# Kernel optimization log

Hardware: AMD Instinct MI355X
Metric: run time of the kernel (lower is better)

## Reference

```python
import math
import jax, jax.numpy as jnp
import numpy as np

B, S, H, N = 2, 2048, 1024, 16
HN = H // N
ALPHA = 32.0


def setup_inputs() -> dict:
    key = jax.random.key(0)
    k1, k2, k3, k4, k5 = jax.random.split(key, 5)
    hidden_states = jax.random.normal(k1, (B, S, H), dtype=jnp.float32)
    # lower-triangular causal mask, broadcastable over batch and heads
    ltor_mask = jnp.tril(jnp.ones((S, S), dtype=jnp.float32))[None, None]
    w_qkv = jax.random.normal(k2, (H, 3 * H), dtype=jnp.float32) * 0.02
    b_qkv = jax.random.normal(k3, (3 * H,), dtype=jnp.float32) * 0.02
    w_dense = jax.random.normal(k4, (H, H), dtype=jnp.float32) * 0.02
    b_dense = jax.random.normal(k5, (H,), dtype=jnp.float32) * 0.02
    return {"hidden_states": hidden_states, "ltor_mask": ltor_mask,
            "w_qkv": w_qkv, "b_qkv": b_qkv, "w_dense": w_dense, "b_dense": b_dense}


def reference(hidden_states, ltor_mask, w_qkv, b_qkv, w_dense, b_dense):
    b, s, h = hidden_states.shape
    # fused QKV projection, split into q/k/v chunks along last dim
    qkv = hidden_states @ w_qkv + b_qkv            # [b, s, 3h]
    q, k, v = jnp.split(qkv, 3, axis=-1)
    # [b, s, h] -> [b, n, s, hn]
    def heads(t):
        return t.reshape(b, s, N, HN).transpose(0, 2, 1, 3)
    q, k, v = heads(q), heads(k), heads(v)
    # pb-relax: scale q before the matmul
    scores = jnp.einsum('bnqd,bnkd->bnqk', q / math.sqrt(HN), k)  # [b, n, s, s]
    mask = ltor_mask[:, :, -s:]                    # [1, 1, s, s]
    scores = scores * mask - 10000.0 * (1.0 - mask)
    # pb-relax max-subtraction stabilization (max over both score dims per head)
    ss = scores / ALPHA
    m = jax.lax.stop_gradient(jnp.max(ss.reshape(b, N, -1), axis=-1))[:, :, None, None]
    scores = (ss - m) * ALPHA
    probs = jax.nn.softmax(scores, axis=-1)        # dropout prob = 0
    ctx = jnp.einsum('bnqk,bnkd->bnqd', probs, v)  # [b, n, s, hn]
    ctx = ctx.transpose(0, 2, 1, 3).reshape(b, s, h)
    out = ctx @ w_dense + b_dense
    return out
```

## Files before the change

### kernel.cpp

```cpp
#include <hip/hip_runtime.h>
#include <hip/hip_bf16.h>
#include <stdint.h>

#define BB 2
#define SS 2048
#define HH 1024

typedef unsigned short u16;
typedef uint32_t u32;
typedef short bf8v __attribute__((ext_vector_type(8)));
typedef float f4 __attribute__((ext_vector_type(4)));

__device__ __forceinline__ u16 f2bf(float f) {
    u32 u = __builtin_bit_cast(u32, f);
    u = (u + 0x7fffu + ((u >> 16) & 1u)) >> 16;
    return (u16)u;
}

__device__ __forceinline__ void async16(const void* g, void* lds) {
    __builtin_amdgcn_global_load_lds(
        (const __attribute__((address_space(1))) u32*)g,
        (__attribute__((address_space(3))) u32*)lds, 16, 0, 0);
}

__device__ __forceinline__ bf8v lds8(const u16* base, int byteoff) {
    return *(const bf8v*)((const char*)base + byteoff);
}

__global__ void cast_f32_bf16(const float* __restrict__ in, u16* __restrict__ out, int n) {
    int i = (blockIdx.x * blockDim.x + threadIdx.x) * 4;
    if (i < n) {
        float4 v = *(const float4*)(in + i);
        ushort4 o;
        o.x = f2bf(v.x); o.y = f2bf(v.y); o.z = f2bf(v.z); o.w = f2bf(v.w);
        *(ushort4*)(out + i) = o;
    }
}

__global__ void transpose_cast(const float* __restrict__ w, u16* __restrict__ wt, int K, int Nn) {
    __shared__ float tile[32][33];
    int tn = blockIdx.x, tk = blockIdx.y;
    int c = threadIdx.x & 31, r0 = threadIdx.x >> 5;
#pragma unroll
    for (int it = 0; it < 4; ++it) {
        int r = r0 + it * 8;
        tile[r][c] = w[(size_t)(tk * 32 + r) * Nn + tn * 32 + c];
    }
    __syncthreads();
#pragma unroll
    for (int it = 0; it < 4; ++it) {
        int r = r0 + it * 8;
        wt[(size_t)(tn * 32 + r) * K + tk * 32 + c] = f2bf(tile[c][r]);
    }
}

template<int EPI>
__global__ __launch_bounds__(256) void gemm_bt(
    const u16* __restrict__ A, const u16* __restrict__ Bt,
    const float* __restrict__ bias, void* __restrict__ Cout,
    int M, int N, int K)
{
    __shared__ __align__(16) u16 As[128 * 64];
    __shared__ __align__(16) u16 Bs[128 * 64];
    const int m0 = blockIdx.y * 128, n0 = blockIdx.x * 128;
    const int t = threadIdx.x, w = t >> 6, l = t & 63;
    const int wr = w >> 1, wc = w & 1;

    f4 acc[4][4];
#pragma unroll
    for (int i = 0; i < 4; ++i)
#pragma unroll
        for (int j = 0; j < 4; ++j) acc[i][j] = (f4){0.f, 0.f, 0.f, 0.f};

    const int nk = K >> 6;
    for (int kt = 0; kt < nk; ++kt) {
        const int k0 = kt << 6;
#pragma unroll
        for (int i = 0; i < 4; ++i) {
            int chunk = w * 256 + i * 64 + l;
            int row = chunk >> 3, seg = chunk & 7;
            int segg = seg ^ (row & 7);
            async16(A + (size_t)(m0 + row) * K + k0 + segg * 8,
                    (char*)As + (w * 256 + i * 64) * 16);
        }
#pragma unroll
        for (int i = 0; i < 4; ++i) {
            int chunk = w * 256 + i * 64 + l;
            int row = chunk >> 3, seg = chunk & 7;
            int segg = seg ^ (row & 7);
            async16(Bt + (size_t)(n0 + row) * K + k0 + segg * 8,
                    (char*)Bs + (w * 256 + i * 64) * 16);
        }
        __syncthreads();
#pragma unroll
        for (int kk = 0; kk < 2; ++kk) {
            bf8v af[4], bq[4];
#pragma unroll
            for (int fq = 0; fq < 4; ++fq) {
                int row = wr * 64 + fq * 16 + (l & 15);
                af[fq] = lds8(As, (row * 128 + kk * 64 + ((l >> 4) * 16)) ^ ((row & 7) << 4));
            }
#pragma unroll
            for (int fr = 0; fr < 4; ++fr) {
                int row = wc * 64 + fr * 16 + (l & 15);
                bq[fr] = lds8(Bs, (row * 128 + kk * 64 + ((l >> 4) * 16)) ^ ((row & 7) << 4));
            }
#pragma unroll
            for (int fq = 0; fq < 4; ++fq)
#pragma unroll
                for (int fr = 0; fr < 4; ++fr)
                    acc[fq][fr] = __builtin_amdgcn_mfma_f32_16x16x32_bf16(
                        af[fq], bq[fr], acc[fq][fr], 0, 0, 0);
        }
        __syncthreads();
    }
#pragma unroll
    for (int fq = 0; fq < 4; ++fq) {
#pragma unroll
        for (int fr = 0; fr < 4; ++fr) {
            int col = n0 + wc * 64 + fr * 16 + (l & 15);
            float bv = bias[col];
#pragma unroll
            for (int j = 0; j < 4; ++j) {
                int row = m0 + wr * 64 + fq * 16 + ((l >> 4) * 4) + j;
                float v = acc[fq][fr][j] + bv;
                if (EPI == 0) {
                    if (col < HH) v *= 0.125f;
                    ((u16*)Cout)[(size_t)row * N + col] = f2bf(v);
                } else {
                    ((float*)Cout)[(size_t)row * N + col] = v;
                }
            }
        }
    }
}

__global__ __launch_bounds__(256) void attn_kernel(
    const u16* __restrict__ qkv,
    u16* __restrict__ ctx)
{
    __shared__ __align__(16) u16 Ks[2][64 * 64];
    __shared__ __align__(16) u16 Vt[2][64 * 64];
    __shared__ __align__(16) u16 Ps[4][16 * 64];

    const int bid = blockIdx.x;
    const int head = (bid & 7) * 4 + (bid >> 7);
    const int p    = (bid >> 3) & 15;
    const int b = head >> 4, n = head & 15;
    const int w = threadIdx.x >> 6, l = threadIdx.x & 63;
    const size_t rs = 3072;

    const int qtA = p, qtB = 31 - p;
    const int ntA = qtA + 1;
    const int S_TOT = 33;

    const u16* kb0 = qkv + (size_t)(b * SS) * rs + HH + n * 64;
    const u16* vb0 = qkv + (size_t)(b * SS) * rs + 2 * HH + n * 64;

    bf8v qA0, qA1, qB0, qB1;
    {
        const u16* qa_ = qkv + (size_t)(b * SS + qtA * 64 + w * 16 + (l & 15)) * rs + n * 64;
        qA0 = *(const bf8v*)(qa_ + ((l >> 4) * 8));
        qA1 = *(const bf8v*)(qa_ + 32 + ((l >> 4) * 8));
        const u16* qb_ = qkv + (size_t)(b * SS + qtB * 64 + w * 16 + (l & 15)) * rs + n * 64;
        qB0 = *(const bf8v*)(qb_ + ((l >> 4) * 8));
        qB1 = *(const bf8v*)(qb_ + 32 + ((l >> 4) * 8));
    }

    auto stageK = [&](int kt, int buf) {
#pragma unroll
        for (int i = 0; i < 2; ++i) {
            int cbase = w * 128 + i * 64;
            int chunk = cbase + l;
            int row = chunk >> 3, seg = chunk & 7;
            int segg = seg ^ (row & 7);
            async16(kb0 + (size_t)(kt * 64 + row) * rs + segg * 8,
                    (char*)Ks[buf] + cbase * 16);
        }
    };
    auto loadV = [&](int kt, bf8v& v0, bf8v& v1) {
        const u16* vp = vb0 + (size_t)(kt * 64 + l) * rs + w * 16;
        v0 = *(const bf8v*)vp;
        v1 = *(const bf8v*)(vp + 8);
    };
    auto writeVt = [&](int buf, bf8v v0, bf8v v1) {
#pragma unroll
        for (int j = 0; j < 8; ++j) {
            int d = w * 16 + j;
            int a = (d * 128 + l * 2) ^ ((d & 7) << 4);
            *(u16*)((char*)Vt[buf] + a) = (u16)v0[j];
        }
#pragma unroll
        for (int j = 0; j < 8; ++j) {
            int d = w * 16 + 8 + j;
            int a = (d * 128 + l * 2) ^ ((d & 7) << 4);
            *(u16*)((char*)Vt[buf] + a) = (u16)v1[j];
        }
    };

    {
        bf8v v0c, v1c;
        stageK(0, 0);
        loadV(0, v0c, v1c);
        writeVt(0, v0c, v1c);
    }
    __syncthreads();

    const int q16 = l & 15;

    for (int phase = 0; phase < 2; ++phase) {
        const int qt = phase ? qtB : qtA;
        const int nt = phase ? (S_TOT - ntA) : ntA;
        const int sbase = phase ? ntA : 0;
        const bf8v q0 = phase ? qB0 : qA0;
        const bf8v q1 = phase ? qB1 : qA1;

        f4 o[4];
#pragma unroll
        for (int od = 0; od < 4; ++od) o[od] = (f4){0.f, 0.f, 0.f, 0.f};
        float lsum = 0.f;

        for (int kt = 0; kt < nt; ++kt) {
            const int s = sbase + kt;
            const int cur = s & 1, nx = cur ^ 1;
            const bool pf = (s + 1 < S_TOT);
            bf8v v0n, v1n;
            if (pf) {
                const int s2 = s + 1;
                const int kt2 = (s2 >= ntA) ? (s2 - ntA) : s2;
                stageK(kt2, nx);
                loadV(kt2, v0n, v1n);
            }

            f4 sf[4];
#pragma unroll
            for (int fr = 0; fr < 4; ++fr) sf[fr] = (f4){0.f, 0.f, 0.f, 0.f};
            __builtin_amdgcn_s_setprio(1);
#pragma unroll
            for (int fr = 0; fr < 4; ++fr) {
                int row = fr * 16 + q16;
                bf8v kf0 = lds8(Ks[cur], (row * 128 + ((l >> 4) * 16)) ^ ((row & 7) << 4));
                bf8v kf1 = lds8(Ks[cur], (row * 128 + 64 + ((l >> 4) * 16)) ^ ((row & 7) << 4));
                sf[fr] = __builtin_amdgcn_mfma_f32_16x16x32_bf16(kf0, q0, sf[fr], 0, 0, 0);
                sf[fr] = __builtin_amdgcn_mfma_f32_16x16x32_bf16(kf1, q1, sf[fr], 0, 0, 0);
            }
            __builtin_amdgcn_s_setprio(0);

            const bool diag = (kt == qt);
            const int qloc = w * 16 + q16;
            float rsumL = 0.f;
#pragma unroll
            for (int fr = 0; fr < 4; ++fr) {
                float pv[4];
#pragma unroll
                for (int j = 0; j < 4; ++j) {
                    float pe = __expf(sf[fr][j]);
                    if (diag && (fr * 16 + ((l >> 4) * 4) + j > qloc)) pe = 0.f;
                    pv[j] = pe;
                    rsumL += pe;
                }
                u32 lo = (u32)f2bf(pv[0]) | ((u32)f2bf(pv[1]) << 16);
                u32 hi = (u32)f2bf(pv[2]) | ((u32)f2bf(pv[3]) << 16);
                int a = (q16 * 128 + fr * 32 + ((l >> 4) * 8)) ^ ((q16 & 7) << 4);
                *(uint2*)((char*)Ps[w] + a) = make_uint2(lo, hi);
            }
            rsumL += __shfl_xor(rsumL, 16);
            rsumL += __shfl_xor(rsumL, 32);
            lsum += rsumL;

            __builtin_amdgcn_s_setprio(1);
#pragma unroll
            for (int kk = 0; kk < 2; ++kk) {
                bf8v pa = lds8(Ps[w], (q16 * 128 + kk * 64 + ((l >> 4) * 16)) ^ ((q16 & 7) << 4));
#pragma unroll
                for (int od = 0; od < 4; ++od) {
                    int drow = od * 16 + q16;
                    bf8v vf = lds8(Vt[cur],
                                   (drow * 128 + kk * 64 + ((l >> 4) * 16)) ^ ((drow & 7) << 4));
                    o[od] = __builtin_amdgcn_mfma_f32_16x16x32_bf16(pa, vf, o[od], 0, 0, 0);
                }
            }
            __builtin_amdgcn_s_setprio(0);

            if (pf) writeVt(nx, v0n, v1n);
            __syncthreads();
        }

        u16* cb = ctx + (size_t)(b * SS + qt * 64 + w * 16) * HH + n * 64;
#pragma unroll
        for (int j = 0; j < 4; ++j) {
            int qrow = ((l >> 4) * 4) + j;
            float inv = 1.0f / __shfl(lsum, qrow);
#pragma unroll
            for (int od = 0; od < 4; ++od) {
                int d = od * 16 + q16;
                cb[(size_t)qrow * HH + d] = f2bf(o[od][j] * inv);
            }
        }
    }
}

extern "C" void kernel_launch(void* const* d_in, const int* in_sizes, int n_in,
                              void* d_out, int out_size, void* d_ws, size_t ws_size,
                              hipStream_t stream)
{
    const float* hidden  = (const float*)d_in[0];
    const float* w_qkv   = (const float*)d_in[2];
    const float* b_qkv   = (const float*)d_in[3];
    const float* w_dense = (const float*)d_in[4];
    const float* b_dense = (const float*)d_in[5];

    u16* hid_bf = (u16*)d_ws;
    u16* wqkvT  = hid_bf + (size_t)4096 * 1024;
    u16* wdT    = wqkvT  + (size_t)3072 * 1024;
    u16* qkv_bf = wdT    + (size_t)1024 * 1024;
    u16* ctx_bf = hid_bf;

    cast_f32_bf16<<<4096, 256, 0, stream>>>(hidden, hid_bf, 4096 * 1024);
    transpose_cast<<<dim3(96, 32), 256, 0, stream>>>(w_qkv, wqkvT, 1024, 3072);
    transpose_cast<<<dim3(32, 32), 256, 0, stream>>>(w_dense, wdT, 1024, 1024);

    gemm_bt<0><<<dim3(24, 32), 256, 0, stream>>>(hid_bf, wqkvT, b_qkv, qkv_bf,
                                                 4096, 3072, 1024);
    attn_kernel<<<512, 256, 0, stream>>>(qkv_bf, ctx_bf);
    gemm_bt<1><<<dim3(8, 32), 256, 0, stream>>>(ctx_bf, wdT, b_dense, d_out,
                                                4096, 1024, 1024);
}
```

Baseline: 219.2 us.

## Fold log2e into Q scale, pack V transpose writes, precompute LDS offsets

```diff
diff --git a/kernel.cpp b/kernel.cpp
--- a/kernel.cpp
+++ b/kernel.cpp
@@ -11,20 +11,22 @@
 typedef short bf8v __attribute__((ext_vector_type(8)));
 typedef float f4 __attribute__((ext_vector_type(4)));
 
+#define QSCALE 0.18033688011112042f
+
 __device__ __forceinline__ u16 f2bf(float f) {
     u32 u = __builtin_bit_cast(u32, f);
     u = (u + 0x7fffu + ((u >> 16) & 1u)) >> 16;
     return (u16)u;
 }
 
+__device__ __forceinline__ u16 bfbits(float f) {
+    return __builtin_bit_cast(u16, __float2bfloat16(f));
+}
+
 __device__ __forceinline__ void async16(const void* g, void* lds) {
     __builtin_amdgcn_global_load_lds(
         (const __attribute__((address_space(1))) u32*)g,
         (__attribute__((address_space(3))) u32*)lds, 16, 0, 0);
-}
-
-__device__ __forceinline__ bf8v lds8(const u16* base, int byteoff) {
-    return *(const bf8v*)((const char*)base + byteoff);
 }
 
 __global__ void cast_f32_bf16(const float* __restrict__ in, u16* __restrict__ out, int n) {
@@ -98,12 +100,14 @@
 #pragma unroll
             for (int fq = 0; fq < 4; ++fq) {
                 int row = wr * 64 + fq * 16 + (l & 15);
-                af[fq] = lds8(As, (row * 128 + kk * 64 + ((l >> 4) * 16)) ^ ((row & 7) << 4));
+                af[fq] = *(const bf8v*)((const char*)As +
+                    ((row * 128 + kk * 64 + ((l >> 4) * 16)) ^ ((row & 7) << 4)));
             }
 #pragma unroll
             for (int fr = 0; fr < 4; ++fr) {
                 int row = wc * 64 + fr * 16 + (l & 15);
-                bq[fr] = lds8(Bs, (row * 128 + kk * 64 + ((l >> 4) * 16)) ^ ((row & 7) << 4));
+                bq[fr] = *(const bf8v*)((const char*)Bs +
+                    ((row * 128 + kk * 64 + ((l >> 4) * 16)) ^ ((row & 7) << 4)));
             }
 #pragma unroll
             for (int fq = 0; fq < 4; ++fq)
@@ -125,7 +129,7 @@
                 int row = m0 + wr * 64 + fq * 16 + ((l >> 4) * 4) + j;
                 float v = acc[fq][fr][j] + bv;
                 if (EPI == 0) {
-                    if (col < HH) v *= 0.125f;
+                    if (col < HH) v *= QSCALE;
                     ((u16*)Cout)[(size_t)row * N + col] = f2bf(v);
                 } else {
                     ((float*)Cout)[(size_t)row * N + col] = v;
@@ -135,37 +139,39 @@
     }
 }
 
-__global__ __launch_bounds__(256) void attn_kernel(
+__global__ __launch_bounds__(256, 2) void attn_kernel(
     const u16* __restrict__ qkv,
     u16* __restrict__ ctx)
 {
-    __shared__ __align__(16) u16 Ks[2][64 * 64];
-    __shared__ __align__(16) u16 Vt[2][64 * 64];
-    __shared__ __align__(16) u16 Ps[4][16 * 64];
+    __shared__ __align__(16) char sm[40960];
 
     const int bid = blockIdx.x;
     const int head = (bid & 7) * 4 + (bid >> 7);
     const int p    = (bid >> 3) & 15;
     const int b = head >> 4, n = head & 15;
     const int w = threadIdx.x >> 6, l = threadIdx.x & 63;
+    const int q16 = l & 15, hi = l >> 4;
     const size_t rs = 3072;
 
     const int qtA = p, qtB = 31 - p;
     const int ntA = qtA + 1;
-    const int S_TOT = 33;
 
     const u16* kb0 = qkv + (size_t)(b * SS) * rs + HH + n * 64;
     const u16* vb0 = qkv + (size_t)(b * SS) * rs + 2 * HH + n * 64;
 
-    bf8v qA0, qA1, qB0, qB1;
-    {
-        const u16* qa_ = qkv + (size_t)(b * SS + qtA * 64 + w * 16 + (l & 15)) * rs + n * 64;
-        qA0 = *(const bf8v*)(qa_ + ((l >> 4) * 8));
-        qA1 = *(const bf8v*)(qa_ + 32 + ((l >> 4) * 8));
-        const u16* qb_ = qkv + (size_t)(b * SS + qtB * 64 + w * 16 + (l & 15)) * rs + n * 64;
-        qB0 = *(const bf8v*)(qb_ + ((l >> 4) * 8));
-        qB1 = *(const bf8v*)(qb_ + 32 + ((l >> 4) * 8));
-    }
+    const int m_   = (q16 & 7) << 4;
+    const int krd0 = (q16 * 128 + hi * 16) ^ m_;
+    const int krd1 = (q16 * 128 + 64 + hi * 16) ^ m_;
+    const int psw  = 32768 + w * 2048;
+    const int par0 = psw + krd0, par1 = psw + krd1;
+    const int pstb = psw + q16 * 128;
+    const int pst0 = pstb + ((0  + hi * 8) ^ m_);
+    const int pst1 = pstb + ((32 + hi * 8) ^ m_);
+    const int pst2 = pstb + ((64 + hi * 8) ^ m_);
+    const int pst3 = pstb + ((96 + hi * 8) ^ m_);
+    const int vwb  = 16384 + w * 2048 + (l >> 5) * 1024;
+    const int vwl  = (l & 31) * 4;
+    const int vrow2 = (l & 31) * 2, vcol = w * 16 + (l >> 5) * 8;
 
     auto stageK = [&](int kt, int buf) {
 #pragma unroll
@@ -175,45 +181,42 @@
             int row = chunk >> 3, seg = chunk & 7;
             int segg = seg ^ (row & 7);
             async16(kb0 + (size_t)(kt * 64 + row) * rs + segg * 8,
-                    (char*)Ks[buf] + cbase * 16);
+                    sm + buf * 8192 + cbase * 16);
         }
     };
     auto loadV = [&](int kt, bf8v& v0, bf8v& v1) {
-        const u16* vp = vb0 + (size_t)(kt * 64 + l) * rs + w * 16;
+        const u16* vp = vb0 + (size_t)(kt * 64 + vrow2) * rs + vcol;
         v0 = *(const bf8v*)vp;
-        v1 = *(const bf8v*)(vp + 8);
+        v1 = *(const bf8v*)(vp + rs);
     };
     auto writeVt = [&](int buf, bf8v v0, bf8v v1) {
+        char* base = sm + vwb + buf * 8192;
 #pragma unroll
         for (int j = 0; j < 8; ++j) {
-            int d = w * 16 + j;
-            int a = (d * 128 + l * 2) ^ ((d & 7) << 4);
-            *(u16*)((char*)Vt[buf] + a) = (u16)v0[j];
-        }
-#pragma unroll
-        for (int j = 0; j < 8; ++j) {
-            int d = w * 16 + 8 + j;
-            int a = (d * 128 + l * 2) ^ ((d & 7) << 4);
-            *(u16*)((char*)Vt[buf] + a) = (u16)v1[j];
+            u32 pk = (u32)(u16)v0[j] | ((u32)(u16)v1[j] << 16);
+            *(u32*)(base + j * 128 + (vwl ^ (j << 4))) = pk;
         }
     };
 
     {
+        stageK(0, 0);
         bf8v v0c, v1c;
-        stageK(0, 0);
         loadV(0, v0c, v1c);
         writeVt(0, v0c, v1c);
     }
     __syncthreads();
 
-    const int q16 = l & 15;
-
     for (int phase = 0; phase < 2; ++phase) {
         const int qt = phase ? qtB : qtA;
-        const int nt = phase ? (S_TOT - ntA) : ntA;
+        const int nt = phase ? (33 - ntA) : ntA;
         const int sbase = phase ? ntA : 0;
-        const bf8v q0 = phase ? qB0 : qA0;
-        const bf8v q1 = phase ? qB1 : qA1;
+
+        bf8v q0, q1;
+        {
+            const u16* qp = qkv + (size_t)(b * SS + qt * 64 + w * 16 + q16) * rs + n * 64;
+            q0 = *(const bf8v*)(qp + hi * 8);
+            q1 = *(const bf8v*)(qp + 32 + hi * 8);
+        }
 
         f4 o[4];
 #pragma unroll
@@ -223,14 +226,17 @@
         for (int kt = 0; kt < nt; ++kt) {
             const int s = sbase + kt;
             const int cur = s & 1, nx = cur ^ 1;
-            const bool pf = (s + 1 < S_TOT);
-            bf8v v0n, v1n;
+            const bool pf = (s + 1 < 33);
+            bf8v nv0, nv1;
             if (pf) {
                 const int s2 = s + 1;
                 const int kt2 = (s2 >= ntA) ? (s2 - ntA) : s2;
                 stageK(kt2, nx);
-                loadV(kt2, v0n, v1n);
-            }
+                loadV(kt2, nv0, nv1);
+            }
+
+            const int ka0 = krd0 + (cur << 13);
+            const int ka1 = krd1 + (cur << 13);
 
             f4 sf[4];
 #pragma unroll
@@ -238,58 +244,71 @@
             __builtin_amdgcn_s_setprio(1);
 #pragma unroll
             for (int fr = 0; fr < 4; ++fr) {
-                int row = fr * 16 + q16;
-                bf8v kf0 = lds8(Ks[cur], (row * 128 + ((l >> 4) * 16)) ^ ((row & 7) << 4));
-                bf8v kf1 = lds8(Ks[cur], (row * 128 + 64 + ((l >> 4) * 16)) ^ ((row & 7) << 4));
+                bf8v kf0 = *(const bf8v*)(sm + ka0 + fr * 2048);
+                bf8v kf1 = *(const bf8v*)(sm + ka1 + fr * 2048);
                 sf[fr] = __builtin_amdgcn_mfma_f32_16x16x32_bf16(kf0, q0, sf[fr], 0, 0, 0);
                 sf[fr] = __builtin_amdgcn_mfma_f32_16x16x32_bf16(kf1, q1, sf[fr], 0, 0, 0);
             }
             __builtin_amdgcn_s_setprio(0);
 
-            const bool diag = (kt == qt);
-            const int qloc = w * 16 + q16;
+            float pv[4][4];
+#pragma unroll
+            for (int fr = 0; fr < 4; ++fr)
+#pragma unroll
+                for (int j = 0; j < 4; ++j) pv[fr][j] = exp2f(sf[fr][j]);
+            if (kt == nt - 1) {
+                const int qloc = w * 16 + q16;
+#pragma unroll
+                for (int fr = 0; fr < 4; ++fr)
+#pragma unroll
+                    for (int j = 0; j < 4; ++j)
+                        if (fr * 16 + hi * 4 + j > qloc) pv[fr][j] = 0.f;
+            }
             float rsumL = 0.f;
 #pragma unroll
-            for (int fr = 0; fr < 4; ++fr) {
-                float pv[4];
-#pragma unroll
-                for (int j = 0; j < 4; ++j) {
-                    float pe = __expf(sf[fr][j]);
-                    if (diag && (fr * 16 + ((l >> 4) * 4) + j > qloc)) pe = 0.f;
-                    pv[j] = pe;
-                    rsumL += pe;
-                }
-                u32 lo = (u32)f2bf(pv[0]) | ((u32)f2bf(pv[1]) << 16);
-                u32 hi = (u32)f2bf(pv[2]) | ((u32)f2bf(pv[3]) << 16);
-                int a = (q16 * 128 + fr * 32 + ((l >> 4) * 8)) ^ ((q16 & 7) << 4);
-                *(uint2*)((char*)Ps[w] + a) = make_uint2(lo, hi);
-            }
+            for (int fr = 0; fr < 4; ++fr)
+#pragma unroll
+                for (int j = 0; j < 4; ++j) rsumL += pv[fr][j];
             rsumL += __shfl_xor(rsumL, 16);
             rsumL += __shfl_xor(rsumL, 32);
             lsum += rsumL;
 
+            {
+                u32 a0 = (u32)bfbits(pv[0][0]) | ((u32)bfbits(pv[0][1]) << 16);
+                u32 a1 = (u32)bfbits(pv[0][2]) | ((u32)bfbits(pv[0][3]) << 16);
+                *(uint2*)(sm + pst0) = make_uint2(a0, a1);
+                u32 b0 = (u32)bfbits(pv[1][0]) | ((u32)bfbits(pv[1][1]) << 16);
+                u32 b1 = (u32)bfbits(pv[1][2]) | ((u32)bfbits(pv[1][3]) << 16);
+                *(uint2*)(sm + pst1) = make_uint2(b0, b1);
+                u32 c0 = (u32)bfbits(pv[2][0]) | ((u32)bfbits(pv[2][1]) << 16);
+                u32 c1 = (u32)bfbits(pv[2][2]) | ((u32)bfbits(pv[2][3]) << 16);
+                *(uint2*)(sm + pst2) = make_uint2(c0, c1);
+                u32 d0 = (u32)bfbits(pv[3][0]) | ((u32)bfbits(pv[3][1]) << 16);
+                u32 d1 = (u32)bfbits(pv[3][2]) | ((u32)bfbits(pv[3][3]) << 16);
+                *(uint2*)(sm + pst3) = make_uint2(d0, d1);
+            }
+
             __builtin_amdgcn_s_setprio(1);
 #pragma unroll
             for (int kk = 0; kk < 2; ++kk) {
-                bf8v pa = lds8(Ps[w], (q16 * 128 + kk * 64 + ((l >> 4) * 16)) ^ ((q16 & 7) << 4));
+                bf8v pa = *(const bf8v*)(sm + (kk ? par1 : par0));
+                const int kab = (kk ? ka1 : ka0) + 16384;
 #pragma unroll
                 for (int od = 0; od < 4; ++od) {
-                    int drow = od * 16 + q16;
-                    bf8v vf = lds8(Vt[cur],
-                                   (drow * 128 + kk * 64 + ((l >> 4) * 16)) ^ ((drow & 7) << 4));
+                    bf8v vf = *(const bf8v*)(sm + kab + od * 2048);
                     o[od] = __builtin_amdgcn_mfma_f32_16x16x32_bf16(pa, vf, o[od], 0, 0, 0);
                 }
             }
             __builtin_amdgcn_s_setprio(0);
 
-            if (pf) writeVt(nx, v0n, v1n);
+            if (pf) writeVt(nx, nv0, nv1);
             __syncthreads();
         }
 
         u16* cb = ctx + (size_t)(b * SS + qt * 64 + w * 16) * HH + n * 64;
 #pragma unroll
         for (int j = 0; j < 4; ++j) {
-            int qrow = ((l >> 4) * 4) + j;
+            int qrow = hi * 4 + j;
             float inv = 1.0f / __shfl(lsum, qrow);
 #pragma unroll
             for (int od = 0; od < 4; ++od) {
```

Result: no change. 215.8 us (-1.5%).
